# Kernel tuning notes

Measured on AMD Instinct MI355X. Metric: run time of the kernel, lower is better.

The kernel has to match this reference:

```python
import jax, jax.numpy as jnp
import numpy as np

K, Q, DIM = 64, 128, 1024
TF_W, DE_W, FFT_W = 1.0, 0.8, 0.6  # opt.TF_weight / DE_weight / FFT_weight


def setup_inputs() -> dict:
    key = jax.random.key(0)
    ks = jax.random.split(key, 9)
    def feats(k):
        return jax.random.normal(k, (K, Q, DIM), dtype=jnp.float32)
    def protos(k):
        return jax.random.normal(k, (K, DIM), dtype=jnp.float32)
    def var(k):
        # positive variances, bounded away from zero
        return jax.random.uniform(k, (K,), dtype=jnp.float32) + 0.5
    return {
        "TFq_output": feats(ks[0]), "TFs_proto": protos(ks[1]), "TF_variance": var(ks[2]),
        "DEq_output": feats(ks[3]), "DEs_proto": protos(ks[4]), "DE_variance": var(ks[5]),
        "FFTq_output": feats(ks[6]), "FFTs_proto": protos(ks[7]), "FFT_variance": var(ks[8]),
    }


def _mah_dist(xq, proto, variance):
    # ||x - p||^2 / var via expansion: avoids materializing (num, protonum, dim)
    x2 = jnp.sum(xq * xq, axis=1, keepdims=True)            # (num, 1)
    p2 = jnp.sum(proto * proto, axis=1)[None, :]            # (1, protonum)
    xp = xq @ proto.T                                       # (num, protonum)
    return (x2 - 2.0 * xp + p2) / variance[None, :]


def _modality(xq, proto, variance, w):
    logits = -_mah_dist(xq, proto, variance)
    pred = w * jax.nn.softmax(logits, axis=1)
    mahloss = -(w * jax.nn.log_softmax(logits, axis=1))
    return pred, mahloss


def reference(TFq_output, TFs_proto, TF_variance,
              DEq_output, DEs_proto, DE_variance,
              FFTq_output, FFTs_proto, FFT_variance):
    k, q, _ = TFq_output.shape
    y = jnp.repeat(jnp.arange(k), q)                         # (k*q,)

    tf_pred, tf_loss = _modality(TFq_output.reshape(k * q, -1), TFs_proto, TF_variance, TF_W)
    de_pred, de_loss = _modality(DEq_output.reshape(k * q, -1), DEs_proto, DE_variance, DE_W)
    fft_pred, fft_loss = _modality(FFTq_output.reshape(k * q, -1), FFTs_proto, FFT_variance, FFT_W)

    fusion_loss = tf_loss + de_loss + fft_loss               # (k*q, k)
    loss = jnp.take_along_axis(fusion_loss, y[:, None], axis=1).squeeze(-1).mean()

    pred_mah = tf_pred + de_pred + fft_pred
    pred = jnp.argmax(pred_mah, axis=1)
    acc = (pred == y).astype(jnp.float32).mean()
    return (loss, acc)
```

## Files before the change

kernel.cpp:

```cpp
#include <hip/hip_runtime.h>


typedef _Float16 half8 __attribute__((ext_vector_type(8)));
typedef float    floatx4 __attribute__((ext_vector_type(4)));

#define NCLS   64
#define QPC    128
#define DIM    1024
#define NROWS  (NCLS * QPC)
#define NRT    (NROWS / 16)

#define OFF_W      0
#define W_BYTES    (3 * NCLS * DIM * 2)
#define OFF_P2     W_BYTES
#define OFF_LP     (OFF_P2 + 3 * NCLS * 4)
#define OFF_CP     (OFF_LP + NRT * 4)
#define WS_NEED    (OFF_CP + NRT * 4)

__global__ __launch_bounds__(64) void prep_protos(
    const float* __restrict__ Ptf, const float* __restrict__ Pde,
    const float* __restrict__ Pff, _Float16* __restrict__ W,
    float* __restrict__ p2)
{
    const int m    = blockIdx.x >> 5;
    const int kcg  = blockIdx.x & 31;
    const int lane = threadIdx.x;
    const int l15  = lane & 15;
    const int quad = lane >> 4;
    const float* __restrict__ P = (m == 0) ? Ptf : (m == 1) ? Pde : Pff;

    #pragma unroll
    for (int t = 0; t < 4; ++t) {
        const float* src = P + (size_t)(t * 16 + l15) * DIM + kcg * 32 + quad * 8;
        const float4 b0 = *reinterpret_cast<const float4*>(src);
        const float4 b1 = *reinterpret_cast<const float4*>(src + 4);
        half8 h;
        h[0] = (_Float16)b0.x; h[1] = (_Float16)b0.y;
        h[2] = (_Float16)b0.z; h[3] = (_Float16)b0.w;
        h[4] = (_Float16)b1.x; h[5] = (_Float16)b1.y;
        h[6] = (_Float16)b1.z; h[7] = (_Float16)b1.w;
        *reinterpret_cast<half8*>(W + ((size_t)(m * 32 + kcg) * 4 + t) * 512 + lane * 8) = h;

        float s = b0.x*b0.x + b0.y*b0.y + b0.z*b0.z + b0.w*b0.w
                + b1.x*b1.x + b1.y*b1.y + b1.z*b1.z + b1.w*b1.w;
        s += __shfl_xor(s, 16);
        s += __shfl_xor(s, 32);
        if (quad == 0) atomicAdd(&p2[m * 64 + t * 16 + l15], s);
    }
}

__global__ __launch_bounds__(384, 3) void fusion_all(
    const float* __restrict__ Xtf, const float* __restrict__ Xde,
    const float* __restrict__ Xff,
    const float* __restrict__ Vtf, const float* __restrict__ Vde,
    const float* __restrict__ Vff,
    const _Float16* __restrict__ W, const float* __restrict__ p2g,
    float* __restrict__ lossPart,
    float* __restrict__ cntPart)
{
    __shared__ float cmb[3][17][64];
    __shared__ float x2s[3][16];
    __shared__ float predS[3][16][66];
    __shared__ float lossW[6];
    __shared__ float cntW[4];

    const int tid  = threadIdx.x;
    const int w    = tid >> 6;
    const int lane = tid & 63;
    const int l15  = lane & 15;
    const int quad = lane >> 4;
    const int m    = w >> 1;
    const int h    = w & 1;
    const int rowBase = blockIdx.x * 16;

    const float* __restrict__ X = (m == 0) ? Xtf : (m == 1) ? Xde : Xff;
    const float* __restrict__ V = (m == 0) ? Vtf : (m == 1) ? Vde : Vff;
    const float  wgt = (m == 0) ? 1.0f : (m == 1) ? 0.8f : 0.6f;

    const float* __restrict__ xr =
        X + (size_t)(rowBase + l15) * DIM + h * 512 + quad * 8;
    const _Float16* __restrict__ wb =
        W + ((size_t)(m * 32 + h * 16) * 4) * 512 + lane * 8;

    floatx4 dd[4];
    #pragma unroll
    for (int n = 0; n < 4; ++n) dd[n] = (floatx4){0.f, 0.f, 0.f, 0.f};
    float x2p = 0.0f;

    float4 aA[4], aB[4];
    half8  bf[4][4];

#define FENCE asm volatile("" ::: "memory")

#define ISSUE(S, KC) do {                                                   \
    aA[S] = *reinterpret_cast<const float4*>(xr + (KC) * 32);               \
    aB[S] = *reinterpret_cast<const float4*>(xr + (KC) * 32 + 4);           \
    bf[S][0] = *reinterpret_cast<const half8*>(wb + ((KC)*4 + 0) * 512);    \
    bf[S][1] = *reinterpret_cast<const half8*>(wb + ((KC)*4 + 1) * 512);    \
    bf[S][2] = *reinterpret_cast<const half8*>(wb + ((KC)*4 + 2) * 512);    \
    bf[S][3] = *reinterpret_cast<const half8*>(wb + ((KC)*4 + 3) * 512);    \
} while (0)

#define CONSUME(S) do {                                                     \
    const float4 A0 = aA[S];                                                \
    const float4 A1 = aB[S];                                                \
    x2p += A0.x*A0.x + A0.y*A0.y + A0.z*A0.z + A0.w*A0.w                    \
         + A1.x*A1.x + A1.y*A1.y + A1.z*A1.z + A1.w*A1.w;                   \
    half8 af;                                                               \
    af[0] = (_Float16)A0.x; af[1] = (_Float16)A0.y;                         \
    af[2] = (_Float16)A0.z; af[3] = (_Float16)A0.w;                         \
    af[4] = (_Float16)A1.x; af[5] = (_Float16)A1.y;                         \
    af[6] = (_Float16)A1.z; af[7] = (_Float16)A1.w;                         \
    dd[0] = __builtin_amdgcn_mfma_f32_16x16x32_f16(af, bf[S][0], dd[0],0,0,0); \
    dd[1] = __builtin_amdgcn_mfma_f32_16x16x32_f16(af, bf[S][1], dd[1],0,0,0); \
    dd[2] = __builtin_amdgcn_mfma_f32_16x16x32_f16(af, bf[S][2], dd[2],0,0,0); \
    dd[3] = __builtin_amdgcn_mfma_f32_16x16x32_f16(af, bf[S][3], dd[3],0,0,0); \
} while (0)

#define STEP(J) do {                                                        \
    if ((J) + 3 < 16) { ISSUE(((J) + 3) & 3, (J) + 3); }                    \
    FENCE;                                                                  \
    CONSUME((J) & 3);                                                       \
} while (0)

    ISSUE(0, 0); FENCE;
    ISSUE(1, 1); FENCE;
    ISSUE(2, 2); FENCE;

    STEP(0);  STEP(1);  STEP(2);  STEP(3);
    STEP(4);  STEP(5);  STEP(6);  STEP(7);
    STEP(8);  STEP(9);  STEP(10); STEP(11);
    STEP(12); STEP(13); STEP(14); STEP(15);

#undef STEP
#undef CONSUME
#undef ISSUE
#undef FENCE

    x2p += __shfl_xor(x2p, 16);
    x2p += __shfl_xor(x2p, 32);

    if (h == 1) {
        #pragma unroll
        for (int n = 0; n < 4; ++n)
            #pragma unroll
            for (int r = 0; r < 4; ++r)
                cmb[m][n * 4 + r][lane] = dd[n][r];
        cmb[m][16][lane] = x2p;
    }
    __syncthreads();
    if (h == 0) {
        #pragma unroll
        for (int n = 0; n < 4; ++n)
            #pragma unroll
            for (int r = 0; r < 4; ++r)
                dd[n][r] += cmb[m][n * 4 + r][lane];
        x2p += cmb[m][16][lane];
        if (quad == 0) x2s[m][l15] = x2p;
    }
    __syncthreads();

    const int y = rowBase >> 7;
    float lossAcc = 0.0f;
    if (h == 0) {
        float vc[4], p2c[4];
        #pragma unroll
        for (int n = 0; n < 4; ++n) {
            const int col = n * 16 + l15;
            vc[n]  = V[col];
            p2c[n] = p2g[m * 64 + col];
        }
        #pragma unroll
        for (int r = 0; r < 4; ++r) {
            const int row  = quad * 4 + r;
            const float x2r = x2s[m][row];
            float lg[4];
            float mx = -3.4e38f;
            #pragma unroll
            for (int n = 0; n < 4; ++n) {
                lg[n] = (2.0f * dd[n][r] - x2r - p2c[n]) / vc[n];
                mx = fmaxf(mx, lg[n]);
            }
            #pragma unroll
            for (int dl = 1; dl <= 8; dl <<= 1) mx = fmaxf(mx, __shfl_xor(mx, dl));
            float s = 0.0f;
            #pragma unroll
            for (int n = 0; n < 4; ++n) s += expf(lg[n] - mx);
            #pragma unroll
            for (int dl = 1; dl <= 8; dl <<= 1) s += __shfl_xor(s, dl);
            const float lse = mx + logf(s);
            #pragma unroll
            for (int n = 0; n < 4; ++n) {
                const int col = n * 16 + l15;
                if (col == y) lossAcc += wgt * (lse - lg[n]);
                predS[m][row][col] = wgt * expf(lg[n] - lse);
            }
        }
    }
    #pragma unroll
    for (int dl = 1; dl <= 32; dl <<= 1) lossAcc += __shfl_xor(lossAcc, dl);
    if (lane == 0) lossW[w] = (h == 0) ? lossAcc : 0.0f;
    __syncthreads();

    if (w < 4) {
        float cnt = 0.0f;
        #pragma unroll
        for (int r4 = 0; r4 < 4; ++r4) {
            const int row = w * 4 + r4;
            float bv = predS[0][row][lane] + predS[1][row][lane]
                     + predS[2][row][lane];
            int bc = lane;
            #pragma unroll
            for (int dl = 1; dl <= 32; dl <<= 1) {
                const float ov = __shfl_xor(bv, dl);
                const int   oc = __shfl_xor(bc, dl);
                if (ov > bv || (ov == bv && oc < bc)) { bv = ov; bc = oc; }
            }
            if (bc == y) cnt += 1.0f;
        }
        if (lane == 0) cntW[w] = cnt;
    }
    __syncthreads();

    if (tid == 0) {
        float L = 0.0f;
        #pragma unroll
        for (int i = 0; i < 6; ++i) L += lossW[i];
        lossPart[blockIdx.x] = L;
        cntPart[blockIdx.x]  = cntW[0] + cntW[1] + cntW[2] + cntW[3];
    }
}

__global__ __launch_bounds__(256) void finalize2(
    const float* __restrict__ lossPart, const float* __restrict__ cntPart,
    float* __restrict__ out)
{
    const int tid  = threadIdx.x;
    const int lane = tid & 63;
    const int v    = tid >> 6;
    float l = 0.0f, c = 0.0f;
    for (int i = tid; i < NRT; i += 256) l += lossPart[i];
    for (int i = tid; i < NRT; i += 256) c += cntPart[i];
    #pragma unroll
    for (int dl = 1; dl <= 32; dl <<= 1) {
        l += __shfl_xor(l, dl);
        c += __shfl_xor(c, dl);
    }
    __shared__ float sl[4], sc[4];
    if (lane == 0) { sl[v] = l; sc[v] = c; }
    __syncthreads();
    if (tid == 0) {
        out[0] = (sl[0] + sl[1] + sl[2] + sl[3]) * (1.0f / NROWS);
        out[1] = (sc[0] + sc[1] + sc[2] + sc[3]) * (1.0f / NROWS);
    }
}

#define NWAVES 12
#define KSPLIT 4
#define KSLICE (DIM / KSPLIT)
#define NITER  (KSLICE / 32)
#define DSTRIDE 17
#define PSTRIDE 65

__global__ __launch_bounds__(NWAVES * 64) void fusion_loss_fallback(
    const float* __restrict__ Xtf, const float* __restrict__ Ptf, const float* __restrict__ Vtf,
    const float* __restrict__ Xde, const float* __restrict__ Pde, const float* __restrict__ Vde,
    const float* __restrict__ Xff, const float* __restrict__ Pff, const float* __restrict__ Vff,
    float* __restrict__ out)
{
    __shared__ float dpart[NWAVES][64 * DSTRIDE];
    __shared__ float x2part[NWAVES][16];
    __shared__ float p2part[NWAVES][64];
    __shared__ float predL[16 * PSTRIDE];
    __shared__ float lossL;

    const int tid  = threadIdx.x;
    const int wave = tid >> 6;
    const int lane = tid & 63;
    const int l15  = lane & 15;
    const int quad = lane >> 4;
    const int m    = wave >> 2;
    const int kq   = wave & 3;
    const int rowBase = blockIdx.x * 16;

    for (int i = tid; i < 16 * PSTRIDE; i += NWAVES * 64) predL[i] = 0.0f;
    if (tid == 0) lossL = 0.0f;

    const float* __restrict__ X = (m == 0) ? Xtf : (m == 1) ? Xde : Xff;
    const float* __restrict__ P = (m == 0) ? Ptf : (m == 1) ? Pde : Pff;
    const float* __restrict__ V = (m == 0) ? Vtf : (m == 1) ? Vde : Vff;
    const float  w = (m == 0) ? 1.0f : (m == 1) ? 0.8f : 0.6f;

    floatx4 d[4];
    #pragma unroll
    for (int t = 0; t < 4; ++t) d[t] = (floatx4){0.f, 0.f, 0.f, 0.f};
    float x2p    = 0.0f;
    float p2p[4] = {0.f, 0.f, 0.f, 0.f};

    const float* xrow = X + (size_t)(rowBase + l15) * DIM + kq * KSLICE + quad * 8;
    const float* prow[4];
    #pragma unroll
    for (int t = 0; t < 4; ++t)
        prow[t] = P + (size_t)(t * 16 + l15) * DIM + kq * KSLICE + quad * 8;

    #pragma unroll 2
    for (int kc = 0; kc < NITER; ++kc) {
        const int ko = kc * 32;
        const float4 a0 = *reinterpret_cast<const float4*>(xrow + ko);
        const float4 a1 = *reinterpret_cast<const float4*>(xrow + ko + 4);
        float4 b0[4], b1[4];
        #pragma unroll
        for (int t = 0; t < 4; ++t) {
            b0[t] = *reinterpret_cast<const float4*>(prow[t] + ko);
            b1[t] = *reinterpret_cast<const float4*>(prow[t] + ko + 4);
        }
        x2p += a0.x*a0.x + a0.y*a0.y + a0.z*a0.z + a0.w*a0.w
             + a1.x*a1.x + a1.y*a1.y + a1.z*a1.z + a1.w*a1.w;
        half8 af;
        af[0] = (_Float16)a0.x; af[1] = (_Float16)a0.y;
        af[2] = (_Float16)a0.z; af[3] = (_Float16)a0.w;
        af[4] = (_Float16)a1.x; af[5] = (_Float16)a1.y;
        af[6] = (_Float16)a1.z; af[7] = (_Float16)a1.w;
        #pragma unroll
        for (int t = 0; t < 4; ++t) {
            p2p[t] += b0[t].x*b0[t].x + b0[t].y*b0[t].y + b0[t].z*b0[t].z + b0[t].w*b0[t].w
                    + b1[t].x*b1[t].x + b1[t].y*b1[t].y + b1[t].z*b1[t].z + b1[t].w*b1[t].w;
            half8 bf;
            bf[0] = (_Float16)b0[t].x; bf[1] = (_Float16)b0[t].y;
            bf[2] = (_Float16)b0[t].z; bf[3] = (_Float16)b0[t].w;
            bf[4] = (_Float16)b1[t].x; bf[5] = (_Float16)b1[t].y;
            bf[6] = (_Float16)b1[t].z; bf[7] = (_Float16)b1[t].w;
            d[t] = __builtin_amdgcn_mfma_f32_16x16x32_f16(af, bf, d[t], 0, 0, 0);
        }
    }

    x2p += __shfl_xor(x2p, 16);
    x2p += __shfl_xor(x2p, 32);
    #pragma unroll
    for (int t = 0; t < 4; ++t) {
        p2p[t] += __shfl_xor(p2p[t], 16);
        p2p[t] += __shfl_xor(p2p[t], 32);
    }
    {
        float* dp = &dpart[wave][lane * DSTRIDE];
        #pragma unroll
        for (int t = 0; t < 4; ++t)
            *reinterpret_cast<float4*>(dp + t * 4) =
                make_float4(d[t][0], d[t][1], d[t][2], d[t][3]);
        if (quad == 0) {
            x2part[wave][l15] = x2p;
            #pragma unroll
            for (int t = 0; t < 4; ++t) p2part[wave][t * 16 + l15] = p2p[t];
        }
    }
    __syncthreads();

    const int y = rowBase >> 7;

    if (kq == 0) {
        floatx4 dsum[4];
        #pragma unroll
        for (int t = 0; t < 4; ++t) dsum[t] = (floatx4){0.f, 0.f, 0.f, 0.f};
        float x2r[4] = {0.f, 0.f, 0.f, 0.f};
        float p2c[4] = {0.f, 0.f, 0.f, 0.f};
        #pragma unroll
        for (int k2 = 0; k2 < KSPLIT; ++k2) {
            const int wv = m * 4 + k2;
            const float* src = &dpart[wv][lane * DSTRIDE];
            #pragma unroll
            for (int t = 0; t < 4; ++t) {
                const float4 vv = *reinterpret_cast<const float4*>(src + t * 4);
                dsum[t][0] += vv.x; dsum[t][1] += vv.y; dsum[t][2] += vv.z; dsum[t][3] += vv.w;
            }
            #pragma unroll
            for (int r = 0; r < 4; ++r) x2r[r] += x2part[wv][quad * 4 + r];
            #pragma unroll
            for (int t = 0; t < 4; ++t) p2c[t] += p2part[wv][t * 16 + l15];
        }
        float vc[4];
        #pragma unroll
        for (int t = 0; t < 4; ++t) vc[t] = V[t * 16 + l15];

        float lossAcc = 0.0f;
        #pragma unroll
        for (int r = 0; r < 4; ++r) {
            float lg[4];
            #pragma unroll
            for (int t = 0; t < 4; ++t)
                lg[t] = (2.0f * dsum[t][r] - x2r[r] - p2c[t]) / vc[t];
            float mx = fmaxf(fmaxf(lg[0], lg[1]), fmaxf(lg[2], lg[3]));
            #pragma unroll
            for (int dl = 1; dl <= 8; dl <<= 1) mx = fmaxf(mx, __shfl_xor(mx, dl));
            float s = expf(lg[0] - mx) + expf(lg[1] - mx)
                    + expf(lg[2] - mx) + expf(lg[3] - mx);
            #pragma unroll
            for (int dl = 1; dl <= 8; dl <<= 1) s += __shfl_xor(s, dl);
            const float lse = mx + logf(s);
            const int row = quad * 4 + r;
            #pragma unroll
            for (int t = 0; t < 4; ++t) {
                const int colc = t * 16 + l15;
                if (colc == y) lossAcc += w * (lse - lg[t]);
                atomicAdd(&predL[row * PSTRIDE + colc], w * expf(lg[t] - lse));
            }
        }
        #pragma unroll
        for (int dl = 1; dl <= 32; dl <<= 1) lossAcc += __shfl_xor(lossAcc, dl);
        if (lane == 0) atomicAdd(&lossL, lossAcc);
    }
    __syncthreads();

    if (wave == 0) {
        float cnt = 0.0f;
        #pragma unroll 1
        for (int r = 0; r < 16; ++r) {
            float bv = predL[r * PSTRIDE + lane];
            int   bc = lane;
            #pragma unroll
            for (int dl = 1; dl <= 32; dl <<= 1) {
                const float ov = __shfl_xor(bv, dl);
                const int   oc = __shfl_xor(bc, dl);
                if (ov > bv || (ov == bv && oc < bc)) { bv = ov; bc = oc; }
            }
            if (lane == 0 && bc == y) cnt += 1.0f;
        }
        if (lane == 0) {
            atomicAdd(&out[0], lossL * (1.0f / NROWS));
            atomicAdd(&out[1], cnt * (1.0f / NROWS));
        }
    }
}

extern "C" void kernel_launch(void* const* d_in, const int* in_sizes, int n_in,
                              void* d_out, int out_size, void* d_ws, size_t ws_size,
                              hipStream_t stream) {
    const float* Xtf = (const float*)d_in[0];
    const float* Ptf = (const float*)d_in[1];
    const float* Vtf = (const float*)d_in[2];
    const float* Xde = (const float*)d_in[3];
    const float* Pde = (const float*)d_in[4];
    const float* Vde = (const float*)d_in[5];
    const float* Xff = (const float*)d_in[6];
    const float* Pff = (const float*)d_in[7];
    const float* Vff = (const float*)d_in[8];
    float* out = (float*)d_out;

    if (ws_size >= (size_t)WS_NEED) {
        char* ws = (char*)d_ws;
        _Float16* W     = (_Float16*)(ws + OFF_W);
        float*    p2    = (float*)(ws + OFF_P2);
        float*    lossP = (float*)(ws + OFF_LP);
        float*    cntP  = (float*)(ws + OFF_CP);

        hipMemsetAsync(p2, 0, 3 * NCLS * sizeof(float), stream);
        prep_protos<<<dim3(96), dim3(64), 0, stream>>>(Ptf, Pde, Pff, W, p2);
        fusion_all<<<dim3(NRT), dim3(384), 0, stream>>>(
            Xtf, Xde, Xff, Vtf, Vde, Vff, W, p2, lossP, cntP);
        finalize2<<<dim3(1), dim3(256), 0, stream>>>(lossP, cntP, out);
    } else {
        hipMemsetAsync(out, 0, 2 * sizeof(float), stream);
        fusion_loss_fallback<<<dim3(NROWS / 16), dim3(NWAVES * 64), 0, stream>>>(
            Xtf, Ptf, Vtf, Xde, Pde, Vde, Xff, Pff, Vff, out);
    }
}
```

Measured before the change: 151.9 us.

## Stage X tiles through LDS with async global_load_lds ring buffer

Replaces the direct register loads of the fp32 query rows with asynchronous global-to-LDS DMA into a per-wave 4-slot swizzled ring. Each step then reads its A fragment back with ds_read_b128, gated by hand-tuned vmcnt waits. Weight fragments stay in registers, now prefetched two steps ahead instead of three. The aim is to cut VGPR pressure and get coalesced row-contiguous global reads, at the cost of 48KB extra LDS per block (which may hurt occupancy at 3 blocks/CU) and fragile manual waitcnt accounting.

```diff
diff --git a/kernel.cpp b/kernel.cpp
--- a/kernel.cpp
+++ b/kernel.cpp
@@ -16,6 +16,16 @@
 #define OFF_LP     (OFF_P2 + 3 * NCLS * 4)
 #define OFF_CP     (OFF_LP + NRT * 4)
 #define WS_NEED    (OFF_CP + NRT * 4)
+
+__device__ __forceinline__ void dma16(const float* g, float* l) {
+    __builtin_amdgcn_global_load_lds(
+        (const __attribute__((address_space(1))) void*)g,
+        (__attribute__((address_space(3))) void*)l,
+        16, 0, 0);
+}
+
+#define STR_(x) #x
+#define STR(x) STR_(x)
 
 __global__ __launch_bounds__(64) void prep_protos(
     const float* __restrict__ Ptf, const float* __restrict__ Pde,
@@ -58,6 +68,7 @@
     float* __restrict__ lossPart,
     float* __restrict__ cntPart)
 {
+    __shared__ __align__(16) float ring[6][4][512];
     __shared__ float cmb[3][17][64];
     __shared__ float x2s[3][16];
     __shared__ float predS[3][16][66];
@@ -77,64 +88,89 @@
     const float* __restrict__ V = (m == 0) ? Vtf : (m == 1) ? Vde : Vff;
     const float  wgt = (m == 0) ? 1.0f : (m == 1) ? 0.8f : 0.6f;
 
-    const float* __restrict__ xr =
-        X + (size_t)(rowBase + l15) * DIM + h * 512 + quad * 8;
+    const int lr   = lane >> 3;
+    const int lc   = (lane & 7) * 4;
+    const int cSwz = lc ^ (lr * 4);
+    const float* __restrict__ bx0 =
+        X + (size_t)(rowBase + lr) * DIM + h * 512 + cSwz;
+    const float* __restrict__ bx1 =
+        X + (size_t)(rowBase + 8 + lr) * DIM + h * 512 + cSwz;
+
     const _Float16* __restrict__ wb =
         W + ((size_t)(m * 32 + h * 16) * 4) * 512 + lane * 8;
 
+    const int swR = (l15 & 7) * 4;
+    const unsigned ringBase = (unsigned)(unsigned long long)
+        (__attribute__((address_space(3))) char*)&ring[w][0][0];
+    const unsigned va0 = ringBase +
+        (unsigned)((l15 * 32 + ((quad * 8) ^ swR)) * 4);
+    const unsigned va1 = ringBase +
+        (unsigned)((l15 * 32 + (((quad * 8) + 4) ^ swR)) * 4);
+
     floatx4 dd[4];
     #pragma unroll
     for (int n = 0; n < 4; ++n) dd[n] = (floatx4){0.f, 0.f, 0.f, 0.f};
     float x2p = 0.0f;
-
-    float4 aA[4], aB[4];
-    half8  bf[4][4];
+    half8 bReg[4][4];
 
 #define FENCE asm volatile("" ::: "memory")
 
-#define ISSUE(S, KC) do {                                                   \
-    aA[S] = *reinterpret_cast<const float4*>(xr + (KC) * 32);               \
-    aB[S] = *reinterpret_cast<const float4*>(xr + (KC) * 32 + 4);           \
-    bf[S][0] = *reinterpret_cast<const half8*>(wb + ((KC)*4 + 0) * 512);    \
-    bf[S][1] = *reinterpret_cast<const half8*>(wb + ((KC)*4 + 1) * 512);    \
-    bf[S][2] = *reinterpret_cast<const half8*>(wb + ((KC)*4 + 2) * 512);    \
-    bf[S][3] = *reinterpret_cast<const half8*>(wb + ((KC)*4 + 3) * 512);    \
+#define LOADB(K) do {                                                        \
+    bReg[(K) & 3][0] = *reinterpret_cast<const half8*>(wb + ((K)*4 + 0)*512);\
+    bReg[(K) & 3][1] = *reinterpret_cast<const half8*>(wb + ((K)*4 + 1)*512);\
+    bReg[(K) & 3][2] = *reinterpret_cast<const half8*>(wb + ((K)*4 + 2)*512);\
+    bReg[(K) & 3][3] = *reinterpret_cast<const half8*>(wb + ((K)*4 + 3)*512);\
 } while (0)
 
-#define CONSUME(S) do {                                                     \
-    const float4 A0 = aA[S];                                                \
-    const float4 A1 = aB[S];                                                \
-    x2p += A0.x*A0.x + A0.y*A0.y + A0.z*A0.z + A0.w*A0.w                    \
-         + A1.x*A1.x + A1.y*A1.y + A1.z*A1.z + A1.w*A1.w;                   \
-    half8 af;                                                               \
-    af[0] = (_Float16)A0.x; af[1] = (_Float16)A0.y;                         \
-    af[2] = (_Float16)A0.z; af[3] = (_Float16)A0.w;                         \
-    af[4] = (_Float16)A1.x; af[5] = (_Float16)A1.y;                         \
-    af[6] = (_Float16)A1.z; af[7] = (_Float16)A1.w;                         \
-    dd[0] = __builtin_amdgcn_mfma_f32_16x16x32_f16(af, bf[S][0], dd[0],0,0,0); \
-    dd[1] = __builtin_amdgcn_mfma_f32_16x16x32_f16(af, bf[S][1], dd[1],0,0,0); \
-    dd[2] = __builtin_amdgcn_mfma_f32_16x16x32_f16(af, bf[S][2], dd[2],0,0,0); \
-    dd[3] = __builtin_amdgcn_mfma_f32_16x16x32_f16(af, bf[S][3], dd[3],0,0,0); \
+#define STAGE(K) do {                                                        \
+    dma16(bx0 + (K) * 32, &ring[w][(K) & 3][0]);                             \
+    dma16(bx1 + (K) * 32, &ring[w][(K) & 3][256]);                           \
 } while (0)
 
-#define STEP(J) do {                                                        \
-    if ((J) + 3 < 16) { ISSUE(((J) + 3) & 3, (J) + 3); }                    \
-    FENCE;                                                                  \
-    CONSUME((J) & 3);                                                       \
+#define KSTEP(J, VN) do {                                                    \
+    if ((J) + 2 < 16) LOADB((J) + 2);                                        \
+    FENCE;                                                                   \
+    if ((J) + 3 < 16) STAGE((J) + 3);                                        \
+    FENCE;                                                                   \
+    asm volatile("s_waitcnt vmcnt(" STR(VN) ")" ::: "memory");               \
+    __builtin_amdgcn_sched_barrier(0);                                       \
+    float4 a0, a1;                                                           \
+    {                                                                        \
+        const unsigned vA = va0 + ((J) & 3) * 2048u;                         \
+        const unsigned vB = va1 + ((J) & 3) * 2048u;                         \
+        asm volatile("ds_read_b128 %0, %2\n\t"                               \
+                     "ds_read_b128 %1, %3\n\t"                               \
+                     "s_waitcnt lgkmcnt(0)"                                  \
+                     : "=v"(a0), "=v"(a1) : "v"(vA), "v"(vB) : "memory");    \
+    }                                                                        \
+    __builtin_amdgcn_sched_barrier(0);                                       \
+    x2p += a0.x*a0.x + a0.y*a0.y + a0.z*a0.z + a0.w*a0.w                     \
+         + a1.x*a1.x + a1.y*a1.y + a1.z*a1.z + a1.w*a1.w;                    \
+    half8 af;                                                                \
+    af[0] = (_Float16)a0.x; af[1] = (_Float16)a0.y;                          \
+    af[2] = (_Float16)a0.z; af[3] = (_Float16)a0.w;                          \
+    af[4] = (_Float16)a1.x; af[5] = (_Float16)a1.y;                          \
+    af[6] = (_Float16)a1.z; af[7] = (_Float16)a1.w;                          \
+    dd[0] = __builtin_amdgcn_mfma_f32_16x16x32_f16(af, bReg[(J)&3][0], dd[0],0,0,0); \
+    dd[1] = __builtin_amdgcn_mfma_f32_16x16x32_f16(af, bReg[(J)&3][1], dd[1],0,0,0); \
+    dd[2] = __builtin_amdgcn_mfma_f32_16x16x32_f16(af, bReg[(J)&3][2], dd[2],0,0,0); \
+    dd[3] = __builtin_amdgcn_mfma_f32_16x16x32_f16(af, bReg[(J)&3][3], dd[3],0,0,0); \
 } while (0)
 
-    ISSUE(0, 0); FENCE;
-    ISSUE(1, 1); FENCE;
-    ISSUE(2, 2); FENCE;
-
-    STEP(0);  STEP(1);  STEP(2);  STEP(3);
-    STEP(4);  STEP(5);  STEP(6);  STEP(7);
-    STEP(8);  STEP(9);  STEP(10); STEP(11);
-    STEP(12); STEP(13); STEP(14); STEP(15);
-
-#undef STEP
-#undef CONSUME
-#undef ISSUE
+    STAGE(0); FENCE;
+    LOADB(0); FENCE;
+    STAGE(1); FENCE;
+    LOADB(1); FENCE;
+    STAGE(2); FENCE;
+
+    KSTEP(0, 14);  KSTEP(1, 14);  KSTEP(2, 14);  KSTEP(3, 14);
+    KSTEP(4, 14);  KSTEP(5, 14);  KSTEP(6, 14);  KSTEP(7, 14);
+    KSTEP(8, 14);  KSTEP(9, 14);  KSTEP(10, 14); KSTEP(11, 14);
+    KSTEP(12, 14); KSTEP(13, 12); KSTEP(14, 6);  KSTEP(15, 0);
+
+#undef KSTEP
+#undef STAGE
+#undef LOADB
 #undef FENCE
 
     x2p += __shfl_xor(x2p, 16);
```

New measurement: 158.6 us. 4.4% more time.
